# Optimization experiments

Measured on AMD Instinct MI355X. Metric: run time of the kernel, lower is better.

The kernel has to match this reference:

```python
import jax, jax.numpy as jnp
import numpy as np

HIDDEN = 768
NUM_BLOCKS = 8
BLOCK = HIDDEN // NUM_BLOCKS
BASE_THR, K_DECAY, MIN_THR = 0.01, 20.0, 0.0005


def _threshold(height, width):
    # wavenumber-dependent soft-shrink threshold T(k), shape [H, W//2+1]
    fu = jnp.fft.fftfreq(height, d=1.0).astype(jnp.float32)[:, None]
    fv = jnp.fft.rfftfreq(width, d=1.0).astype(jnp.float32)[None, :]
    k = jnp.sqrt(fu ** 2 + fv ** 2) * max(height, width)
    thr = BASE_THR * jnp.exp(-0.5 * (k / K_DECAY) ** 2)
    return jnp.maximum(thr, MIN_THR)


def setup_inputs() -> dict:
    key = jax.random.key(0)
    kx, k1, k2, k3, k4 = jax.random.split(key, 5)
    scale = 0.02
    x = jax.random.normal(kx, (4, 128, 128, HIDDEN), dtype=jnp.float32)
    w1 = scale * jax.random.normal(k1, (2, NUM_BLOCKS, BLOCK, BLOCK), dtype=jnp.float32)
    b1 = scale * jax.random.normal(k2, (2, NUM_BLOCKS, BLOCK), dtype=jnp.float32)
    w2 = scale * jax.random.normal(k3, (2, NUM_BLOCKS, BLOCK, BLOCK), dtype=jnp.float32)
    b2 = scale * jax.random.normal(k4, (2, NUM_BLOCKS, BLOCK), dtype=jnp.float32)
    return {"x": x, "w1": w1, "b1": b1, "w2": w2, "b2": b2}


def reference(x, w1, b1, w2, b2):
    dtype = x.dtype
    bias = x
    xf = x.astype(jnp.float32)
    B, H, W, C = xf.shape
    Wc = W // 2 + 1
    # rfft2 over spatial dims, orthonormal
    Xc = jnp.fft.rfft2(xf, axes=(1, 2), norm='ortho')
    Xc = Xc.reshape(B, H, Wc, NUM_BLOCKS, BLOCK)
    xr, xi = jnp.real(Xc), jnp.imag(Xc)
    mm = lambda t, w: jnp.einsum('bhwni,nio->bhwno', t, w)
    # complex block-diagonal 2-layer MLP
    o1r = jax.nn.relu(mm(xr, w1[0]) - mm(xi, w1[1]) + b1[0])
    o1i = jax.nn.relu(mm(xi, w1[0]) + mm(xr, w1[1]) + b1[1])
    o2r = mm(o1r, w2[0]) - mm(o1i, w2[1]) + b2[0]
    o2i = mm(o1i, w2[0]) + mm(o1r, w2[1]) + b2[1]
    # soft-shrink on complex magnitude with wavenumber-dependent threshold
    mag = jnp.sqrt(o2r ** 2 + o2i ** 2 + 1e-8)
    thr = _threshold(H, W)[None, :, :, None, None]  # [1,H,Wc,1,1]
    sf = jax.nn.relu(mag - thr) / mag
    Yc = (o2r * sf) + 1j * (o2i * sf)
    Yc = Yc.reshape(B, H, Wc, C)
    y = jnp.fft.irfft2(Yc, s=(H, W), axes=(1, 2), norm='ortho')
    return y.astype(dtype) + bias
```

## Files before the change

### kernel.cpp

```cpp
#include <hip/hip_runtime.h>
#include <hip/hip_bf16.h>
#include <math.h>


#define HD   768
#define NBLK 8
#define HH   128
#define WW   128
#define WC   65
#define NPOS (HH * WC)

constexpr float SC    = 0.08838834764831845f;
constexpr float TWOPI = 6.28318530717958647692f;

constexpr int TM_OFF     = 0;
constexpr int TW_OFF     = 49152;
constexpr int TWI_OFF    = 69632;
constexpr int WF_OFF     = 90112;
constexpr int WF_END_U16 = 679936;
constexpr size_t A_UINTS = (size_t)4 * NPOS * HD;

typedef __attribute__((ext_vector_type(8))) short short8;
typedef __attribute__((ext_vector_type(4))) float f32x4;

#define MFMA __builtin_amdgcn_mfma_f32_16x16x32_bf16

static __device__ inline unsigned short f2bf(float f) {
  __hip_bfloat16 h = __float2bfloat16(f);
  return __builtin_bit_cast(unsigned short, h);
}
static __device__ inline unsigned int pack2(float re, float im) {
  return (unsigned int)f2bf(re) | ((unsigned int)f2bf(im) << 16);
}
static __device__ inline float lo2f(unsigned int u) {
  return __builtin_bit_cast(float, u << 16);
}
static __device__ inline float hi2f(unsigned int u) {
  return __builtin_bit_cast(float, u & 0xffff0000u);
}

__global__ __launch_bounds__(256) void k_prep(const float* __restrict__ w1,
                                              const float* __restrict__ b1,
                                              const float* __restrict__ w2,
                                              const float* __restrict__ b2,
                                              unsigned short* __restrict__ wf,
                                              float* __restrict__ bpk) {
  const int blk = blockIdx.x, t = threadIdx.x;
  if (blk < 16) {
    const int layer = blk >> 3, n = blk & 7;
    const float* w  = layer ? w2 : w1;
    const float* bs = layer ? b2 : b1;
    unsigned short* dst = wf + WF_OFF + (size_t)blk * (72 * 512);
    for (int e = t; e < 72 * 512; e += 256) {
      int f = e >> 9, idx = e & 511;
      int kk = f / 12, nt = f - kk * 12;
      int lane = idx >> 3, j = idx & 7;
      int k  = kk * 32 + (lane >> 4) * 8 + j;
      int cc = nt * 16 + (lane & 15);
      float v;
      if (k < 96) v = (cc < 96) ? w[(size_t)n * 9216 + k * 96 + cc]
                                : w[(size_t)(8 + n) * 9216 + k * 96 + (cc - 96)];
      else        v = (cc < 96) ? -w[(size_t)(8 + n) * 9216 + (k - 96) * 96 + cc]
                                :  w[(size_t)n * 9216 + (k - 96) * 96 + (cc - 96)];
      dst[e] = f2bf(v);
    }
    for (int c = t; c < 192; c += 256)
      bpk[blk * 192 + c] = (c < 96) ? bs[n * 96 + c] : bs[(8 + n) * 96 + (c - 96)];
  } else if (blk == 16) {
    for (int e = t; e < 96 * 512; e += 256) {
      int f = e >> 9, idx = e & 511;
      int part = f >> 5, rem = f & 31, kot = rem >> 2, kk = rem & 3;
      int lane = idx >> 3, j = idx & 7;
      int ko = kot * 16 + (lane & 15);
      int r  = kk * 32 + (lane >> 4) * 8 + j;
      float sn, cs; sincosf((TWOPI / 128.f) * (float)((ko * r) & 127), &sn, &cs);
      float v = (part == 0) ? cs : (part == 1) ? sn : -sn;
      wf[TM_OFF + (size_t)f * 512 + idx] = f2bf(v * SC);
    }
  } else if (blk == 17) {
    for (int e = t; e < 40 * 512; e += 256) {
      int f = e >> 9, idx = e & 511;
      int mt = f >> 2, kk = f & 3;
      int lane = idx >> 3, j = idx & 7;
      int row = mt * 16 + (lane & 15);
      int r   = kk * 32 + (lane >> 4) * 8 + j;
      int kor = (row < 80) ? row : row - 80;
      float sn, cs; sincosf((TWOPI / 128.f) * (float)((kor * r) & 127), &sn, &cs);
      wf[TW_OFF + (size_t)f * 512 + idx] = f2bf((row < 80 ? cs : -sn) * SC);
    }
  } else {
    for (int e = t; e < 40 * 512; e += 256) {
      int f = e >> 9, idx = e & 511;
      int mt = f / 5, kk = f - mt * 5;
      int lane = idx >> 3, j = idx & 7;
      int wr = mt * 16 + (lane & 15);
      int k  = kk * 32 + (lane >> 4) * 8 + j;
      float v = 0.f;
      if (k < 80) {
        int kb = k;
        if (kb <= 64) {
          float sn, cs; sincosf((TWOPI / 128.f) * (float)((wr * kb) & 127), &sn, &cs);
          v = SC * ((kb == 0 || kb == 64) ? 1.f : 2.f) * cs;
        }
      } else {
        int kb = k - 80;
        if (kb >= 1 && kb <= 63) {
          float sn, cs; sincosf((TWOPI / 128.f) * (float)((wr * kb) & 127), &sn, &cs);
          v = -2.f * SC * sn;
        }
      }
      wf[TWI_OFF + (size_t)f * 512 + idx] = f2bf(v);
    }
  }
}

__global__ __launch_bounds__(256) void k_fft_w(const float* __restrict__ x,
                                               unsigned int* __restrict__ A,
                                               const unsigned short* __restrict__ wf) {
  __shared__ unsigned short Xt[64 * 136];
  const int h = blockIdx.x, c0 = blockIdx.y * 64, b = blockIdx.z, t = threadIdx.x;
  const int wv = t >> 6, lane = t & 63, l15 = lane & 15, lg = lane >> 4;
  const float* xp = x + ((size_t)(b * HH + h)) * WW * HD + c0;
  for (int idx = t; idx < 128 * 64; idx += 256) {
    int r = idx >> 6, ch = idx & 63;
    Xt[ch * 136 + r] = f2bf(xp[(size_t)r * HD + ch]);
  }
  __syncthreads();
  const unsigned short* tw = wf + TW_OFF;
  f32x4 acc[10];
#pragma unroll
  for (int m = 0; m < 10; ++m) acc[m] = { 0.f, 0.f, 0.f, 0.f };
#pragma unroll
  for (int kk = 0; kk < 4; ++kk) {
    short8 bq = *(const short8*)&Xt[(wv * 16 + l15) * 136 + kk * 32 + lg * 8];
#pragma unroll
    for (int m = 0; m < 10; ++m) {
      short8 a = *(const short8*)&tw[(size_t)(m * 4 + kk) * 512 + lane * 8];
      acc[m] = MFMA(a, bq, acc[m], 0, 0, 0);
    }
  }
  unsigned int* Ao = A + ((size_t)b * NPOS + h * WC) * HD + c0 + wv * 16 + l15;
#pragma unroll
  for (int q = 0; q < 5; ++q)
#pragma unroll
    for (int r = 0; r < 4; ++r) {
      int ko = q * 16 + lg * 4 + r;
      if (ko <= 64) Ao[(size_t)ko * HD] = pack2(acc[q][r], acc[5 + q][r]);
    }
}

__global__ __launch_bounds__(256) void k_ifft_w(const unsigned int* __restrict__ A,
                                                const unsigned int* __restrict__ Bp,
                                                float* __restrict__ out,
                                                const unsigned short* __restrict__ wf) {
  __shared__ unsigned short Zt[64 * 168];
  const int h = blockIdx.x, c0 = blockIdx.y * 64, b = blockIdx.z, t = threadIdx.x;
  const int wv = t >> 6, lane = t & 63, l15 = lane & 15, lg = lane >> 4;
  const size_t base = ((size_t)b * NPOS + h * WC) * HD + c0;
  for (int idx = t; idx < 65 * 64; idx += 256) {
    int kb = idx >> 6, ch = idx & 63;
    unsigned int uA = A[base + (size_t)kb * HD + ch];
    unsigned int uB = Bp[base + (size_t)kb * HD + ch];
    float re = lo2f(uA) + lo2f(uB);
    float im = hi2f(uA) + hi2f(uB);
    Zt[ch * 168 + kb]      = f2bf(re);
    Zt[ch * 168 + 80 + kb] = (kb == 0 || kb == 64) ? (unsigned short)0 : f2bf(im);
  }
  for (int idx = t; idx < 64 * 32; idx += 256) {
    int ch = idx >> 5, q = idx & 31;
    if (q < 30) {
      int kb = 65 + (q % 15), half = q / 15;
      Zt[ch * 168 + half * 80 + kb] = 0;
    }
  }
  __syncthreads();
  const unsigned short* twi = wf + TWI_OFF;
  f32x4 acc[8];
#pragma unroll
  for (int m = 0; m < 8; ++m) acc[m] = { 0.f, 0.f, 0.f, 0.f };
#pragma unroll
  for (int kk = 0; kk < 5; ++kk) {
    short8 bq = *(const short8*)&Zt[(wv * 16 + l15) * 168 + kk * 32 + lg * 8];
#pragma unroll
    for (int m = 0; m < 8; ++m) {
      short8 a = *(const short8*)&twi[(size_t)(m * 5 + kk) * 512 + lane * 8];
      acc[m] = MFMA(a, bq, acc[m], 0, 0, 0);
    }
  }
#pragma unroll
  for (int m = 0; m < 8; ++m)
#pragma unroll
    for (int r = 0; r < 4; ++r) {
      int wr = m * 16 + lg * 4 + r;
      size_t go = (((size_t)(b * HH + h)) * WW + wr) * HD + c0 + wv * 16 + l15;
      out[go] = acc[m][r];
    }
}

template <int FWD>
static __device__ inline void dft_gemm16(const unsigned short* Rb, const unsigned short* Ib,
                                         const unsigned short* tm, int rt, int cb, int lane,
                                         f32x4* aR, f32x4* aI) {
  const int l15 = lane & 15, lg = lane >> 4;
#pragma unroll
  for (int kkr = 0; kkr < 4; ++kkr) {
    const int r0 = kkr * 32 + lg * 8;
    short8 Ac = *(const short8*)&tm[(size_t)(0 * 32 + rt * 4 + kkr) * 512 + lane * 8];
    short8 As = *(const short8*)&tm[(size_t)(1 * 32 + rt * 4 + kkr) * 512 + lane * 8];
    short8 An = *(const short8*)&tm[(size_t)(2 * 32 + rt * 4 + kkr) * 512 + lane * 8];
#pragma unroll
    for (int c = 0; c < 3; ++c) {
      short8 zr = *(const short8*)&Rb[((cb + c) * 16 + l15) * 136 + r0];
      short8 zi = *(const short8*)&Ib[((cb + c) * 16 + l15) * 136 + r0];
      aR[c] = MFMA(Ac, zr, aR[c], 0, 0, 0);
      if constexpr (FWD) {
        aR[c] = MFMA(As, zi, aR[c], 0, 0, 0);
        aI[c] = MFMA(Ac, zi, aI[c], 0, 0, 0);
        aI[c] = MFMA(An, zr, aI[c], 0, 0, 0);
      } else {
        aR[c] = MFMA(An, zi, aR[c], 0, 0, 0);
        aI[c] = MFMA(Ac, zi, aI[c], 0, 0, 0);
        aI[c] = MFMA(As, zr, aI[c], 0, 0, 0);
      }
    }
  }
}

__global__ __launch_bounds__(1024) void k_mid(const unsigned int* __restrict__ A,
                                              unsigned int* __restrict__ Bp,
                                              const unsigned short* __restrict__ wf,
                                              const float* __restrict__ bpk) {
  __shared__ unsigned short Rb[13312], Ib[13312];
  __shared__ unsigned short WfX[2][12 * 512];
  const int kv = blockIdx.x, n = blockIdx.y, b = blockIdx.z, t = threadIdx.x;
  const int w = t >> 6, lane = t & 63, l15 = lane & 15, lg = lane >> 4;
  const int rt = w >> 1, cb = (w & 1) * 3;
  const size_t pbase = ((size_t)b * NPOS + kv) * HD + n * 96;
  const unsigned short* tm = wf + TM_OFF;
  const unsigned short* wf1 = wf + WF_OFF + (size_t)n * (72 * 512);
  const unsigned short* wf2 = wf + WF_OFF + (size_t)(8 + n) * (72 * 512);

  for (int idx = t; idx < 128 * 96; idx += 1024) {
    int r = idx / 96, ch = idx - r * 96;
    unsigned int u = A[pbase + (size_t)r * (WC * HD) + ch];
    Rb[ch * 136 + r] = (unsigned short)(u & 0xffffu);
    Ib[ch * 136 + r] = (unsigned short)(u >> 16);
  }
  if (t < 768) ((int4*)WfX[0])[t] = ((const int4*)(wf1 + 0 * 12 * 512))[t];
  __syncthreads();

  f32x4 aR[3], aI[3];
#pragma unroll
  for (int c = 0; c < 3; ++c) { aR[c] = {0.f,0.f,0.f,0.f}; aI[c] = {0.f,0.f,0.f,0.f}; }
  dft_gemm16<1>(Rb, Ib, tm, rt, cb, lane, aR, aI);
  if (t < 768) ((int4*)WfX[1])[t] = ((const int4*)(wf1 + 1 * 12 * 512))[t];
  __syncthreads();

#pragma unroll
  for (int c = 0; c < 3; ++c)
#pragma unroll
    for (int r = 0; r < 4; ++r) {
      int row = rt * 16 + lg * 4 + r, ch = (cb + c) * 16 + l15;
      Rb[row * 104 + ch] = f2bf(aR[c][r]);
      Ib[row * 104 + ch] = f2bf(aI[c][r]);
    }
  __syncthreads();

  const int row_a = (rt * 16 + l15) * 104;
  f32x4 acc[6];
#pragma unroll
  for (int i = 0; i < 3; ++i) {
    float bv = bpk[n * 192 + (cb + i) * 16 + l15];
    acc[i] = { bv, bv, bv, bv };
    bv = bpk[n * 192 + (cb + i + 6) * 16 + l15];
    acc[3 + i] = { bv, bv, bv, bv };
  }

#define MLP_PAIR(k0, BUF)                                                        \
  {                                                                              \
    short8 aRf = *(const short8*)&Rb[row_a + (k0) * 32 + lg * 8];                \
    short8 aIf = *(const short8*)&Ib[row_a + (k0) * 32 + lg * 8];                \
    short8 wlo[3], whi[3];                                                       \
    _Pragma("unroll")                                                            \
    for (int i = 0; i < 3; ++i) {                                                \
      wlo[i] = *(const short8*)&(BUF)[(cb + i) * 512 + lane * 8];                \
      whi[i] = *(const short8*)&(BUF)[(cb + i + 6) * 512 + lane * 8];            \
    }                                                                            \
    _Pragma("unroll")                                                            \
    for (int i = 0; i < 3; ++i) {                                                \
      int4 nh = __builtin_bit_cast(int4, whi[i]);                                \
      nh.x ^= 0x80008000; nh.y ^= 0x80008000;                                    \
      nh.z ^= 0x80008000; nh.w ^= 0x80008000;                                    \
      acc[i] = MFMA(aRf, wlo[i], acc[i], 0, 0, 0);                               \
      acc[i] = MFMA(aIf, __builtin_bit_cast(short8, nh), acc[i], 0, 0, 0);       \
      acc[3 + i] = MFMA(aRf, whi[i], acc[3 + i], 0, 0, 0);                       \
      acc[3 + i] = MFMA(aIf, wlo[i], acc[3 + i], 0, 0, 0);                       \
    }                                                                            \
  }

  MLP_PAIR(0, WfX[0]);
  __syncthreads();
  MLP_PAIR(1, WfX[1]);
  if (t < 768) ((int4*)WfX[0])[t] = ((const int4*)(wf1 + 2 * 12 * 512))[t];
  __syncthreads();
  MLP_PAIR(2, WfX[0]);
  if (t < 768) ((int4*)WfX[1])[t] = ((const int4*)(wf2 + 0 * 12 * 512))[t];
  __syncthreads();

#pragma unroll
  for (int i = 0; i < 3; ++i)
#pragma unroll
    for (int r = 0; r < 4; ++r) {
      int row = rt * 16 + lg * 4 + r, ch = (cb + i) * 16 + l15;
      Rb[row * 104 + ch] = f2bf(fmaxf(acc[i][r], 0.f));
      Ib[row * 104 + ch] = f2bf(fmaxf(acc[3 + i][r], 0.f));
    }
  if (t < 768) ((int4*)WfX[0])[t] = ((const int4*)(wf2 + 1 * 12 * 512))[t];
  __syncthreads();

#pragma unroll
  for (int i = 0; i < 3; ++i) {
    float bv = bpk[(8 + n) * 192 + (cb + i) * 16 + l15];
    acc[i] = { bv, bv, bv, bv };
    bv = bpk[(8 + n) * 192 + (cb + i + 6) * 16 + l15];
    acc[3 + i] = { bv, bv, bv, bv };
  }
  MLP_PAIR(0, WfX[1]);
  __syncthreads();
  MLP_PAIR(1, WfX[0]);
  if (t < 768) ((int4*)WfX[1])[t] = ((const int4*)(wf2 + 2 * 12 * 512))[t];
  __syncthreads();
  MLP_PAIR(2, WfX[1]);
  __syncthreads();

#pragma unroll
  for (int r = 0; r < 4; ++r) {
    int ko = rt * 16 + lg * 4 + r;
    float kus = (ko >= 64) ? (float)(ko - 128) : (float)ko;
    float k2v = kus * kus + (float)(kv * kv);
    float thr = fmaxf(0.01f * expf(-0.00125f * k2v), 0.0005f);
#pragma unroll
    for (int i = 0; i < 3; ++i) {
      float mr = acc[i][r], mi = acc[3 + i][r];
      float mag = sqrtf(mr * mr + mi * mi + 1e-8f);
      float sf = fmaxf(mag - thr, 0.f) / mag;
      int ch = (cb + i) * 16 + l15;
      Rb[ch * 136 + ko] = f2bf(mr * sf);
      Ib[ch * 136 + ko] = f2bf(mi * sf);
    }
  }
  __syncthreads();

#pragma unroll
  for (int c = 0; c < 3; ++c) { aR[c] = {0.f,0.f,0.f,0.f}; aI[c] = {0.f,0.f,0.f,0.f}; }
  dft_gemm16<0>(Rb, Ib, tm, rt, cb, lane, aR, aI);
#pragma unroll
  for (int c = 0; c < 3; ++c)
#pragma unroll
    for (int r = 0; r < 4; ++r) {
      int rr = rt * 16 + lg * 4 + r, ch = (cb + c) * 16 + l15;
      Bp[pbase + (size_t)rr * (WC * HD) + ch] = pack2(aR[c][r], aI[c][r]);
    }
#undef MLP_PAIR
}

extern "C" void kernel_launch(void* const* d_in, const int* in_sizes, int n_in,
                              void* d_out, int out_size, void* d_ws, size_t ws_size,
                              hipStream_t stream) {
  const float* x  = (const float*)d_in[0];
  const float* w1 = (const float*)d_in[1];
  const float* b1 = (const float*)d_in[2];
  const float* w2 = (const float*)d_in[3];
  const float* b2 = (const float*)d_in[4];
  float* out = (float*)d_out;
  unsigned int* A  = (unsigned int*)d_ws;
  unsigned int* Bp = A + A_UINTS;

  unsigned short* wf = (unsigned short*)(Bp + A_UINTS);
  float* bpk = (float*)(wf + WF_END_U16);

  k_prep<<<19, 256, 0, stream>>>(w1, b1, w2, b2, wf, bpk);
  k_fft_w<<<dim3(HH, HD / 64, 4), 256, 0, stream>>>(x, A, wf);
  k_mid<<<dim3(WC, NBLK, 4), 1024, 0, stream>>>(A, Bp, wf, bpk);
  k_ifft_w<<<dim3(HH, HD / 64, 4), 256, 0, stream>>>(A, Bp, out, wf);
}
```

Before: 405.8 us.

## Process two frequency columns per k_mid block to reuse DFT and MLP weights

Each k_mid workgroup now handles two adjacent kv columns instead of one, doubling the shared-memory data buffers and the accumulator register arrays. DFT twiddle fragments and MLP weight fragments loaded from LDS are reused across both columns, and the grid shrinks from 65 to 33 blocks in x. The intent is to halve weight and twiddle traffic and barrier overhead per column. In exchange, register pressure rises (acc grows to 12 vectors), LDS use goes up, occupancy drops, and the last block does wasted work on a zero-padded column.

```diff
diff --git a/kernel.cpp b/kernel.cpp
--- a/kernel.cpp
+++ b/kernel.cpp
@@ -209,18 +209,25 @@
     short8 As = *(const short8*)&tm[(size_t)(1 * 32 + rt * 4 + kkr) * 512 + lane * 8];
     short8 An = *(const short8*)&tm[(size_t)(2 * 32 + rt * 4 + kkr) * 512 + lane * 8];
 #pragma unroll
-    for (int c = 0; c < 3; ++c) {
-      short8 zr = *(const short8*)&Rb[((cb + c) * 16 + l15) * 136 + r0];
-      short8 zi = *(const short8*)&Ib[((cb + c) * 16 + l15) * 136 + r0];
-      aR[c] = MFMA(Ac, zr, aR[c], 0, 0, 0);
-      if constexpr (FWD) {
-        aR[c] = MFMA(As, zi, aR[c], 0, 0, 0);
-        aI[c] = MFMA(Ac, zi, aI[c], 0, 0, 0);
-        aI[c] = MFMA(An, zr, aI[c], 0, 0, 0);
-      } else {
-        aR[c] = MFMA(An, zi, aR[c], 0, 0, 0);
-        aI[c] = MFMA(Ac, zi, aI[c], 0, 0, 0);
-        aI[c] = MFMA(As, zr, aI[c], 0, 0, 0);
+    for (int q = 0; q < 2; ++q) {
+      const unsigned short* Rq = Rb + q * 13312;
+      const unsigned short* Iq = Ib + q * 13312;
+#pragma unroll
+      for (int c = 0; c < 3; ++c) {
+        short8 zr = *(const short8*)&Rq[((cb + c) * 16 + l15) * 136 + r0];
+        short8 zi = *(const short8*)&Iq[((cb + c) * 16 + l15) * 136 + r0];
+        f32x4* pR = &aR[q * 3 + c];
+        f32x4* pI = &aI[q * 3 + c];
+        *pR = MFMA(Ac, zr, *pR, 0, 0, 0);
+        if constexpr (FWD) {
+          *pR = MFMA(As, zi, *pR, 0, 0, 0);
+          *pI = MFMA(Ac, zi, *pI, 0, 0, 0);
+          *pI = MFMA(An, zr, *pI, 0, 0, 0);
+        } else {
+          *pR = MFMA(An, zi, *pR, 0, 0, 0);
+          *pI = MFMA(Ac, zi, *pI, 0, 0, 0);
+          *pI = MFMA(As, zr, *pI, 0, 0, 0);
+        }
       }
     }
   }
@@ -230,71 +237,87 @@
                                               unsigned int* __restrict__ Bp,
                                               const unsigned short* __restrict__ wf,
                                               const float* __restrict__ bpk) {
-  __shared__ unsigned short Rb[13312], Ib[13312];
+  __shared__ unsigned short Rb[2 * 13312], Ib[2 * 13312];
   __shared__ unsigned short WfX[2][12 * 512];
-  const int kv = blockIdx.x, n = blockIdx.y, b = blockIdx.z, t = threadIdx.x;
+  const int kv0 = blockIdx.x * 2, n = blockIdx.y, b = blockIdx.z, t = threadIdx.x;
+  const bool two = (kv0 + 1) < WC;
   const int w = t >> 6, lane = t & 63, l15 = lane & 15, lg = lane >> 4;
   const int rt = w >> 1, cb = (w & 1) * 3;
-  const size_t pbase = ((size_t)b * NPOS + kv) * HD + n * 96;
+  const size_t pbase0 = ((size_t)b * NPOS + kv0) * HD + n * 96;
   const unsigned short* tm = wf + TM_OFF;
   const unsigned short* wf1 = wf + WF_OFF + (size_t)n * (72 * 512);
   const unsigned short* wf2 = wf + WF_OFF + (size_t)(8 + n) * (72 * 512);
 
   for (int idx = t; idx < 128 * 96; idx += 1024) {
     int r = idx / 96, ch = idx - r * 96;
-    unsigned int u = A[pbase + (size_t)r * (WC * HD) + ch];
-    Rb[ch * 136 + r] = (unsigned short)(u & 0xffffu);
-    Ib[ch * 136 + r] = (unsigned short)(u >> 16);
+    unsigned int u0 = A[pbase0 + (size_t)r * (WC * HD) + ch];
+    Rb[ch * 136 + r] = (unsigned short)(u0 & 0xffffu);
+    Ib[ch * 136 + r] = (unsigned short)(u0 >> 16);
+    unsigned int u1 = two ? A[pbase0 + HD + (size_t)r * (WC * HD) + ch] : 0u;
+    Rb[13312 + ch * 136 + r] = (unsigned short)(u1 & 0xffffu);
+    Ib[13312 + ch * 136 + r] = (unsigned short)(u1 >> 16);
   }
   if (t < 768) ((int4*)WfX[0])[t] = ((const int4*)(wf1 + 0 * 12 * 512))[t];
   __syncthreads();
 
-  f32x4 aR[3], aI[3];
-#pragma unroll
-  for (int c = 0; c < 3; ++c) { aR[c] = {0.f,0.f,0.f,0.f}; aI[c] = {0.f,0.f,0.f,0.f}; }
+  f32x4 aR[6], aI[6];
+#pragma unroll
+  for (int c = 0; c < 6; ++c) { aR[c] = {0.f,0.f,0.f,0.f}; aI[c] = {0.f,0.f,0.f,0.f}; }
   dft_gemm16<1>(Rb, Ib, tm, rt, cb, lane, aR, aI);
   if (t < 768) ((int4*)WfX[1])[t] = ((const int4*)(wf1 + 1 * 12 * 512))[t];
   __syncthreads();
 
 #pragma unroll
-  for (int c = 0; c < 3; ++c)
-#pragma unroll
-    for (int r = 0; r < 4; ++r) {
-      int row = rt * 16 + lg * 4 + r, ch = (cb + c) * 16 + l15;
-      Rb[row * 104 + ch] = f2bf(aR[c][r]);
-      Ib[row * 104 + ch] = f2bf(aI[c][r]);
-    }
+  for (int q = 0; q < 2; ++q)
+#pragma unroll
+    for (int c = 0; c < 3; ++c)
+#pragma unroll
+      for (int r = 0; r < 4; ++r) {
+        int row = rt * 16 + lg * 4 + r, ch = (cb + c) * 16 + l15;
+        Rb[q * 13312 + row * 104 + ch] = f2bf(aR[q * 3 + c][r]);
+        Ib[q * 13312 + row * 104 + ch] = f2bf(aI[q * 3 + c][r]);
+      }
   __syncthreads();
 
   const int row_a = (rt * 16 + l15) * 104;
-  f32x4 acc[6];
+  float bv0[3], bv1[3];
 #pragma unroll
   for (int i = 0; i < 3; ++i) {
-    float bv = bpk[n * 192 + (cb + i) * 16 + l15];
-    acc[i] = { bv, bv, bv, bv };
-    bv = bpk[n * 192 + (cb + i + 6) * 16 + l15];
-    acc[3 + i] = { bv, bv, bv, bv };
-  }
+    bv0[i] = bpk[n * 192 + (cb + i) * 16 + l15];
+    bv1[i] = bpk[n * 192 + (cb + i + 6) * 16 + l15];
+  }
+  f32x4 acc[12];
+#pragma unroll
+  for (int q = 0; q < 2; ++q)
+#pragma unroll
+    for (int i = 0; i < 3; ++i) {
+      acc[q * 6 + i]     = { bv0[i], bv0[i], bv0[i], bv0[i] };
+      acc[q * 6 + 3 + i] = { bv1[i], bv1[i], bv1[i], bv1[i] };
+    }
 
 #define MLP_PAIR(k0, BUF)                                                        \
   {                                                                              \
-    short8 aRf = *(const short8*)&Rb[row_a + (k0) * 32 + lg * 8];                \
-    short8 aIf = *(const short8*)&Ib[row_a + (k0) * 32 + lg * 8];                \
-    short8 wlo[3], whi[3];                                                       \
+    short8 wlo[3], whi[3], whn[3];                                               \
     _Pragma("unroll")                                                            \
     for (int i = 0; i < 3; ++i) {                                                \
       wlo[i] = *(const short8*)&(BUF)[(cb + i) * 512 + lane * 8];                \
       whi[i] = *(const short8*)&(BUF)[(cb + i + 6) * 512 + lane * 8];            \
-    }                                                                            \
-    _Pragma("unroll")                                                            \
-    for (int i = 0; i < 3; ++i) {                                                \
       int4 nh = __builtin_bit_cast(int4, whi[i]);                                \
       nh.x ^= 0x80008000; nh.y ^= 0x80008000;                                    \
       nh.z ^= 0x80008000; nh.w ^= 0x80008000;                                    \
-      acc[i] = MFMA(aRf, wlo[i], acc[i], 0, 0, 0);                               \
-      acc[i] = MFMA(aIf, __builtin_bit_cast(short8, nh), acc[i], 0, 0, 0);       \
-      acc[3 + i] = MFMA(aRf, whi[i], acc[3 + i], 0, 0, 0);                       \
-      acc[3 + i] = MFMA(aIf, wlo[i], acc[3 + i], 0, 0, 0);                       \
+      whn[i] = __builtin_bit_cast(short8, nh);                                   \
+    }                                                                            \
+    _Pragma("unroll")                                                            \
+    for (int q = 0; q < 2; ++q) {                                                \
+      short8 aRf = *(const short8*)&Rb[q * 13312 + row_a + (k0) * 32 + lg * 8];  \
+      short8 aIf = *(const short8*)&Ib[q * 13312 + row_a + (k0) * 32 + lg * 8];  \
+      _Pragma("unroll")                                                          \
+      for (int i = 0; i < 3; ++i) {                                              \
+        acc[q*6+i]   = MFMA(aRf, wlo[i], acc[q*6+i], 0, 0, 0);                   \
+        acc[q*6+i]   = MFMA(aIf, whn[i], acc[q*6+i], 0, 0, 0);                   \
+        acc[q*6+3+i] = MFMA(aRf, whi[i], acc[q*6+3+i], 0, 0, 0);                 \
+        acc[q*6+3+i] = MFMA(aIf, wlo[i], acc[q*6+3+i], 0, 0, 0);                 \
+      }                                                                          \
     }                                                                            \
   }
 
@@ -308,23 +331,30 @@
   __syncthreads();
 
 #pragma unroll
-  for (int i = 0; i < 3; ++i)
-#pragma unroll
-    for (int r = 0; r < 4; ++r) {
-      int row = rt * 16 + lg * 4 + r, ch = (cb + i) * 16 + l15;
-      Rb[row * 104 + ch] = f2bf(fmaxf(acc[i][r], 0.f));
-      Ib[row * 104 + ch] = f2bf(fmaxf(acc[3 + i][r], 0.f));
-    }
+  for (int i = 0; i < 3; ++i) {
+    bv0[i] = bpk[(8 + n) * 192 + (cb + i) * 16 + l15];
+    bv1[i] = bpk[(8 + n) * 192 + (cb + i + 6) * 16 + l15];
+  }
+#pragma unroll
+  for (int q = 0; q < 2; ++q)
+#pragma unroll
+    for (int i = 0; i < 3; ++i)
+#pragma unroll
+      for (int r = 0; r < 4; ++r) {
+        int row = rt * 16 + lg * 4 + r, ch = (cb + i) * 16 + l15;
+        Rb[q * 13312 + row * 104 + ch] = f2bf(fmaxf(acc[q * 6 + i][r], 0.f));
+        Ib[q * 13312 + row * 104 + ch] = f2bf(fmaxf(acc[q * 6 + 3 + i][r], 0.f));
+      }
   if (t < 768) ((int4*)WfX[0])[t] = ((const int4*)(wf2 + 1 * 12 * 512))[t];
   __syncthreads();
 
 #pragma unroll
-  for (int i = 0; i < 3; ++i) {
-    float bv = bpk[(8 + n) * 192 + (cb + i) * 16 + l15];
-    acc[i] = { bv, bv, bv, bv };
-    bv = bpk[(8 + n) * 192 + (cb + i + 6) * 16 + l15];
-    acc[3 + i] = { bv, bv, bv, bv };
-  }
+  for (int q = 0; q < 2; ++q)
+#pragma unroll
+    for (int i = 0; i < 3; ++i) {
+      acc[q * 6 + i]     = { bv0[i], bv0[i], bv0[i], bv0[i] };
+      acc[q * 6 + 3 + i] = { bv1[i], bv1[i], bv1[i], bv1[i] };
+    }
   MLP_PAIR(0, WfX[1]);
   __syncthreads();
   MLP_PAIR(1, WfX[0]);
@@ -337,30 +367,39 @@
   for (int r = 0; r < 4; ++r) {
     int ko = rt * 16 + lg * 4 + r;
     float kus = (ko >= 64) ? (float)(ko - 128) : (float)ko;
-    float k2v = kus * kus + (float)(kv * kv);
-    float thr = fmaxf(0.01f * expf(-0.00125f * k2v), 0.0005f);
-#pragma unroll
-    for (int i = 0; i < 3; ++i) {
-      float mr = acc[i][r], mi = acc[3 + i][r];
-      float mag = sqrtf(mr * mr + mi * mi + 1e-8f);
-      float sf = fmaxf(mag - thr, 0.f) / mag;
-      int ch = (cb + i) * 16 + l15;
-      Rb[ch * 136 + ko] = f2bf(mr * sf);
-      Ib[ch * 136 + ko] = f2bf(mi * sf);
-    }
-  }
-  __syncthreads();
-
-#pragma unroll
-  for (int c = 0; c < 3; ++c) { aR[c] = {0.f,0.f,0.f,0.f}; aI[c] = {0.f,0.f,0.f,0.f}; }
+#pragma unroll
+    for (int q = 0; q < 2; ++q) {
+      float kvf = (float)(kv0 + q);
+      float k2v = kus * kus + kvf * kvf;
+      float thr = fmaxf(0.01f * expf(-0.00125f * k2v), 0.0005f);
+#pragma unroll
+      for (int i = 0; i < 3; ++i) {
+        float mr = acc[q * 6 + i][r], mi = acc[q * 6 + 3 + i][r];
+        float mag = sqrtf(mr * mr + mi * mi + 1e-8f);
+        float sf = fmaxf(mag - thr, 0.f) / mag;
+        int ch = (cb + i) * 16 + l15;
+        Rb[q * 13312 + ch * 136 + ko] = f2bf(mr * sf);
+        Ib[q * 13312 + ch * 136 + ko] = f2bf(mi * sf);
+      }
+    }
+  }
+  __syncthreads();
+
+#pragma unroll
+  for (int c = 0; c < 6; ++c) { aR[c] = {0.f,0.f,0.f,0.f}; aI[c] = {0.f,0.f,0.f,0.f}; }
   dft_gemm16<0>(Rb, Ib, tm, rt, cb, lane, aR, aI);
 #pragma unroll
-  for (int c = 0; c < 3; ++c)
-#pragma unroll
-    for (int r = 0; r < 4; ++r) {
-      int rr = rt * 16 + lg * 4 + r, ch = (cb + c) * 16 + l15;
-      Bp[pbase + (size_t)rr * (WC * HD) + ch] = pack2(aR[c][r], aI[c][r]);
-    }
+  for (int q = 0; q < 2; ++q) {
+    if (q == 1 && !two) break;
+#pragma unroll
+    for (int c = 0; c < 3; ++c)
+#pragma unroll
+      for (int r = 0; r < 4; ++r) {
+        int rr = rt * 16 + lg * 4 + r, ch = (cb + c) * 16 + l15;
+        Bp[pbase0 + q * HD + (size_t)rr * (WC * HD) + ch] =
+            pack2(aR[q * 3 + c][r], aI[q * 3 + c][r]);
+      }
+  }
 #undef MLP_PAIR
 }
 
@@ -381,6 +420,6 @@
 
   k_prep<<<19, 256, 0, stream>>>(w1, b1, w2, b2, wf, bpk);
   k_fft_w<<<dim3(HH, HD / 64, 4), 256, 0, stream>>>(x, A, wf);
-  k_mid<<<dim3(WC, NBLK, 4), 1024, 0, stream>>>(A, Bp, wf, bpk);
+  k_mid<<<dim3(33, NBLK, 4), 1024, 0, stream>>>(A, Bp, wf, bpk);
   k_ifft_w<<<dim3(HH, HD / 64, 4), 256, 0, stream>>>(A, Bp, out, wf);
 }
```

Result: slower. 423.8 us (+4.4%).
